# Kernel tuning notes

Measured on AMD Instinct MI355X. Metric: run time of the kernel, lower is better.

The kernel has to match this reference:

```python
import jax, jax.numpy as jnp
import numpy as np

HEAD_SIZE = 64

def setup_inputs() -> dict:
    key = jax.random.key(0)
    kx, kq, kk, kv = jax.random.split(key, 4)
    n_embd = 1024
    x = jax.random.normal(kx, (4, 2048, n_embd), dtype=jnp.float32)
    s = 1.0 / np.sqrt(n_embd)
    Wq = jax.random.normal(kq, (HEAD_SIZE, n_embd), dtype=jnp.float32) * s
    Wk = jax.random.normal(kk, (HEAD_SIZE, n_embd), dtype=jnp.float32) * s
    Wv = jax.random.normal(kv, (HEAD_SIZE, n_embd), dtype=jnp.float32) * s
    return {"x": x, "Wq": Wq, "Wk": Wk, "Wv": Wv}

def reference(x, Wq, Wk, Wv):
    # x: [B, T, C]; W*: [head_size, C] (torch nn.Linear weight layout, y = x @ W.T)
    B, T, C = x.shape
    q = jnp.einsum('btc,hc->bth', x, Wq)  # [B, T, H]
    k = jnp.einsum('btc,hc->bth', x, Wk)
    v = jnp.einsum('btc,hc->bth', x, Wv)
    att = jnp.einsum('bqh,bkh->bqk', q, k) / jnp.sqrt(jnp.float32(HEAD_SIZE))
    causal = jnp.tril(jnp.ones((T, T), dtype=bool))  # [T, T]
    att = jnp.where(causal, att, -jnp.inf)
    att = jax.nn.softmax(att, axis=-1)
    out = jnp.einsum('bqk,bkh->bqh', att, v)  # [B, T, H]
    return out
```

## Files before the change

### kernel.cpp

```cpp
#include <hip/hip_runtime.h>
#include <hip/hip_bf16.h>

#define NB 4
#define TT 2048
#define CC 1024
#define HS 64
#define L2E 1.4426950408889634f

typedef __attribute__((ext_vector_type(8))) short short8;
typedef __attribute__((ext_vector_type(4))) short short4v;
typedef __attribute__((ext_vector_type(4))) float floatx4;
typedef __attribute__((ext_vector_type(2))) float floatx2;

__device__ __forceinline__ short f2bf(float f) {
  union { float f; unsigned u; } x; x.f = f;
  unsigned r = (x.u + 0x7fffu + ((x.u >> 16) & 1u)) >> 16;
  return (short)r;
}

__device__ __forceinline__ short8 pack_bf16x8(floatx4 a, floatx4 b) {
  union { __hip_bfloat162 h[4]; short8 s; } u;
  u.h[0] = __float22bfloat162_rn(make_float2(a[0], a[1]));
  u.h[1] = __float22bfloat162_rn(make_float2(a[2], a[3]));
  u.h[2] = __float22bfloat162_rn(make_float2(b[0], b[1]));
  u.h[3] = __float22bfloat162_rn(make_float2(b[2], b[3]));
  return u.s;
}

__global__ __launch_bounds__(768) void qkv_proj(const float* __restrict__ x,
                                                const float* __restrict__ wq,
                                                const float* __restrict__ wk,
                                                const float* __restrict__ wv,
                                                short* __restrict__ qb,
                                                short* __restrict__ kbuf,
                                                short* __restrict__ vtb) {
  __shared__ __align__(16) short xs[32 * 1024];
  const int tid  = threadIdx.x;
  const int lane = tid & 63;
  const int w    = tid >> 6;
  const int col  = lane & 15;
  const int quad = lane >> 4;
  const int row32 = blockIdx.x * 32;

  const int mat = w >> 2;
  const int ht  = w & 3;
  const float* wsrc = (mat == 0 ? wq : (mat == 1 ? wk : wv))
                      + (size_t)(ht * 16 + col) * CC + quad * 8;

  floatx4 wa = *(const floatx4*)(wsrc);
  floatx4 wc = *(const floatx4*)(wsrc + 4);

#pragma unroll
  for (int i = 0; i < 6; ++i) {
    int c = i * 768 + tid;
    if (c < 4096) {
      int r = c >> 7;
      int k = (c & 127) * 8;
      const float* src = x + (size_t)(row32 + r) * CC + k;
      floatx4 a = *(const floatx4*)src;
      floatx4 b = *(const floatx4*)(src + 4);
      int kb = k >> 5, ko = k & 31;
      *(short8*)(&xs[kb * 1024 + r * 32 + ko]) = pack_bf16x8(a, b);
    }
  }
  __syncthreads();

  floatx4 acc0 = (floatx4){0.f, 0.f, 0.f, 0.f};
  floatx4 acc1 = (floatx4){0.f, 0.f, 0.f, 0.f};

#pragma unroll
  for (int kb = 0; kb < 32; ++kb) {
    short8 bf = pack_bf16x8(wa, wc);
    if (kb < 31) {
      wa = *(const floatx4*)(wsrc + (kb + 1) * 32);
      wc = *(const floatx4*)(wsrc + (kb + 1) * 32 + 4);
    }
    short8 a0 = *(const short8*)(&xs[kb * 1024 + col * 32 + quad * 8]);
    short8 a1 = *(const short8*)(&xs[kb * 1024 + (16 + col) * 32 + quad * 8]);
    acc0 = __builtin_amdgcn_mfma_f32_16x16x32_bf16(a0, bf, acc0, 0, 0, 0);
    acc1 = __builtin_amdgcn_mfma_f32_16x16x32_bf16(a1, bf, acc1, 0, 0, 0);
  }

  const int h = ht * 16 + col;
  if (mat == 2) {
    int b = row32 >> 11;
    int t = (row32 & (TT - 1)) + quad * 4;
    short4v o;
    o[0] = f2bf(acc0[0]); o[1] = f2bf(acc0[1]); o[2] = f2bf(acc0[2]); o[3] = f2bf(acc0[3]);
    *(short4v*)(vtb + (size_t)(b * HS + h) * TT + t) = o;
    o[0] = f2bf(acc1[0]); o[1] = f2bf(acc1[1]); o[2] = f2bf(acc1[2]); o[3] = f2bf(acc1[3]);
    *(short4v*)(vtb + (size_t)(b * HS + h) * TT + t + 16) = o;
  } else {
    short* dst = (mat == 0) ? qb : kbuf;
    float s = (mat == 0) ? 0.125f : 1.0f;
#pragma unroll
    for (int r = 0; r < 4; ++r) {
      dst[(size_t)(row32 + quad * 4 + r) * HS + h]      = f2bf(acc0[r] * s);
      dst[(size_t)(row32 + 16 + quad * 4 + r) * HS + h] = f2bf(acc1[r] * s);
    }
  }
}

#define PST 72

__global__ __launch_bounds__(512) void attn(const short* __restrict__ qb,
                                            const short* __restrict__ kb,
                                            const short* __restrict__ vtb,
                                            float* __restrict__ out) {
  __shared__ __align__(16) short pt[8][2][16 * PST];
  __shared__ float cl[8][16];
  __shared__ __align__(16) float co[8][16][64];

  const int tid  = threadIdx.x;
  const int lane = tid & 63;
  const int w    = tid >> 6;
  const int col  = lane & 15;
  const int quad = lane >> 4;
  const int b  = blockIdx.x >> 7;
  const int qt = blockIdx.x & 127;
  const int t0 = qt * 16;

  const short* qbase = qb + (size_t)(b * TT + t0) * HS;
  const short* kbase = kb + (size_t)b * TT * HS;
  const short* vbase = vtb + (size_t)b * HS * TT;

  short8 qf0 = *(const short8*)(qbase + col * HS + quad * 8);
  short8 qf1 = *(const short8*)(qbase + col * HS + 32 + quad * 8);

  floatx4 oacc[4];
#pragma unroll
  for (int i = 0; i < 4; ++i) oacc[i] = (floatx4){0.f, 0.f, 0.f, 0.f};
  float lsum[4] = {0.f, 0.f, 0.f, 0.f};

  const int Nc = (t0 + 16 + 63) >> 6;

  int parity = 0;
  for (int c = w; c < Nc; c += 8, parity ^= 1) {
    const int kb0 = c * 64;
    const short* kp = kbase + (size_t)kb0 * HS + quad * 8;

    floatx4 st[4];
#pragma unroll
    for (int j = 0; j < 4; ++j) st[j] = (floatx4){0.f, 0.f, 0.f, 0.f};
#pragma unroll
    for (int j = 0; j < 4; ++j) {
      short8 kfa = *(const short8*)(kp + (size_t)(j * 16 + col) * HS);
      short8 kfb = *(const short8*)(kp + (size_t)(j * 16 + col) * HS + 32);
      st[j] = __builtin_amdgcn_mfma_f32_16x16x32_bf16(qf0, kfa, st[j], 0, 0, 0);
      st[j] = __builtin_amdgcn_mfma_f32_16x16x32_bf16(qf1, kfb, st[j], 0, 0, 0);
    }

    if (kb0 + 63 > t0) {
#pragma unroll
      for (int j = 0; j < 4; ++j) {
        int kcol = kb0 + j * 16 + col;
#pragma unroll
        for (int r = 0; r < 4; ++r)
          if (kcol > t0 + quad * 4 + r) st[j][r] = -1e30f;
      }
    }

    float pv[4][4];
#pragma unroll
    for (int j = 0; j < 4; ++j)
#pragma unroll
      for (int r = 0; r < 4; ++r)
        pv[j][r] = exp2f(st[j][r] * L2E);
#pragma unroll
    for (int r = 0; r < 4; ++r)
      lsum[r] += (pv[0][r] + pv[1][r]) + (pv[2][r] + pv[3][r]);

    short* pw = &pt[w][parity][0];
#pragma unroll
    for (int j = 0; j < 4; ++j)
#pragma unroll
      for (int r = 0; r < 4; ++r)
        pw[(quad * 4 + r) * PST + j * 16 + col] = f2bf(pv[j][r]);
    short8 af0 = *(const short8*)(pw + col * PST + quad * 8);
    short8 af1 = *(const short8*)(pw + col * PST + 32 + quad * 8);

#pragma unroll
    for (int ht = 0; ht < 4; ++ht) {
      const short* vp = vbase + (size_t)(ht * 16 + col) * TT + kb0 + quad * 8;
      short8 vf0 = *(const short8*)(vp);
      short8 vf1 = *(const short8*)(vp + 32);
      oacc[ht] = __builtin_amdgcn_mfma_f32_16x16x32_bf16(af0, vf0, oacc[ht], 0, 0, 0);
      oacc[ht] = __builtin_amdgcn_mfma_f32_16x16x32_bf16(af1, vf1, oacc[ht], 0, 0, 0);
    }
  }

#pragma unroll
  for (int r = 0; r < 4; ++r) {
#pragma unroll
    for (int off = 8; off; off >>= 1) lsum[r] += __shfl_xor(lsum[r], off);
    if (col == 0) cl[w][quad * 4 + r] = lsum[r];
#pragma unroll
    for (int ht = 0; ht < 4; ++ht)
      co[w][quad * 4 + r][ht * 16 + col] = oacc[ht][r];
  }
  __syncthreads();

  const int crow = tid >> 5;
  const int ch   = (tid & 31) << 1;
  float L = 0.f;
  floatx2 a = (floatx2){0.f, 0.f};
#pragma unroll
  for (int w2 = 0; w2 < 8; ++w2) {
    L += cl[w2][crow];
    floatx2 ov = *(const floatx2*)&co[w2][crow][ch];
    a[0] += ov[0]; a[1] += ov[1];
  }
  float inv = 1.0f / L;
  floatx2 res = (floatx2){a[0] * inv, a[1] * inv};
  *(floatx2*)(out + (size_t)(b * TT + t0 + crow) * HS + ch) = res;
}

extern "C" void kernel_launch(void* const* d_in, const int* in_sizes, int n_in,
                              void* d_out, int out_size, void* d_ws, size_t ws_size,
                              hipStream_t stream) {
  const float* x  = (const float*)d_in[0];
  const float* wq = (const float*)d_in[1];
  const float* wk = (const float*)d_in[2];
  const float* wv = (const float*)d_in[3];
  float* out = (float*)d_out;

  char* ws = (char*)d_ws;
  short* qbf = (short*)ws;
  short* kbf = (short*)(ws + 1048576);
  short* vtb = (short*)(ws + 2097152);

  hipLaunchKernelGGL(qkv_proj, dim3(256), dim3(768), 0, stream,
                     x, wq, wk, wv, qbf, kbf, vtb);
  hipLaunchKernelGGL(attn, dim3(512), dim3(512), 0, stream, qbf, kbf, vtb, out);
}
```

Measured before the change: 131.0 us.

## Retile QKV projection to 16-row blocks with padded LDS layout

```diff
diff --git a/kernel.cpp b/kernel.cpp
--- a/kernel.cpp
+++ b/kernel.cpp
@@ -27,40 +27,46 @@
   return u.s;
 }
 
-__global__ __launch_bounds__(768) void qkv_proj(const float* __restrict__ x,
+#define XRS 40
+#define XKS 656
+
+__global__ __launch_bounds__(384) void qkv_proj(const float* __restrict__ x,
                                                 const float* __restrict__ wq,
                                                 const float* __restrict__ wk,
                                                 const float* __restrict__ wv,
                                                 short* __restrict__ qb,
                                                 short* __restrict__ kbuf,
                                                 short* __restrict__ vtb) {
-  __shared__ __align__(16) short xs[32 * 1024];
+  __shared__ __align__(16) short xs[32 * XKS];
   const int tid  = threadIdx.x;
   const int lane = tid & 63;
   const int w    = tid >> 6;
   const int col  = lane & 15;
   const int quad = lane >> 4;
-  const int row32 = blockIdx.x * 32;
-
-  const int mat = w >> 2;
-  const int ht  = w & 3;
-  const float* wsrc = (mat == 0 ? wq : (mat == 1 ? wk : wv))
-                      + (size_t)(ht * 16 + col) * CC + quad * 8;
-
-  floatx4 wa = *(const floatx4*)(wsrc);
-  floatx4 wc = *(const floatx4*)(wsrc + 4);
+  const int row16 = blockIdx.x * 16;
+
+  const int mat = w >> 1;
+  const int hp  = w & 1;
+  const float* wmat = (mat == 0 ? wq : (mat == 1 ? wk : wv));
+  const float* wsrc0 = wmat + (size_t)(hp * 32 + col) * CC + quad * 8;
+  const float* wsrc1 = wmat + (size_t)(hp * 32 + 16 + col) * CC + quad * 8;
+
+  floatx4 wa0 = *(const floatx4*)(wsrc0);
+  floatx4 wc0 = *(const floatx4*)(wsrc0 + 4);
+  floatx4 wa1 = *(const floatx4*)(wsrc1);
+  floatx4 wc1 = *(const floatx4*)(wsrc1 + 4);
 
 #pragma unroll
   for (int i = 0; i < 6; ++i) {
-    int c = i * 768 + tid;
-    if (c < 4096) {
+    int c = i * 384 + tid;
+    if (c < 2048) {
       int r = c >> 7;
       int k = (c & 127) * 8;
-      const float* src = x + (size_t)(row32 + r) * CC + k;
+      const float* src = x + (size_t)(row16 + r) * CC + k;
       floatx4 a = *(const floatx4*)src;
       floatx4 b = *(const floatx4*)(src + 4);
       int kb = k >> 5, ko = k & 31;
-      *(short8*)(&xs[kb * 1024 + r * 32 + ko]) = pack_bf16x8(a, b);
+      *(short8*)(&xs[kb * XKS + r * XRS + ko]) = pack_bf16x8(a, b);
     }
   }
   __syncthreads();
@@ -70,33 +76,36 @@
 
 #pragma unroll
   for (int kb = 0; kb < 32; ++kb) {
-    short8 bf = pack_bf16x8(wa, wc);
+    short8 bf0 = pack_bf16x8(wa0, wc0);
+    short8 bf1 = pack_bf16x8(wa1, wc1);
     if (kb < 31) {
-      wa = *(const floatx4*)(wsrc + (kb + 1) * 32);
-      wc = *(const floatx4*)(wsrc + (kb + 1) * 32 + 4);
-    }
-    short8 a0 = *(const short8*)(&xs[kb * 1024 + col * 32 + quad * 8]);
-    short8 a1 = *(const short8*)(&xs[kb * 1024 + (16 + col) * 32 + quad * 8]);
-    acc0 = __builtin_amdgcn_mfma_f32_16x16x32_bf16(a0, bf, acc0, 0, 0, 0);
-    acc1 = __builtin_amdgcn_mfma_f32_16x16x32_bf16(a1, bf, acc1, 0, 0, 0);
-  }
-
-  const int h = ht * 16 + col;
+      wa0 = *(const floatx4*)(wsrc0 + (kb + 1) * 32);
+      wc0 = *(const floatx4*)(wsrc0 + (kb + 1) * 32 + 4);
+      wa1 = *(const floatx4*)(wsrc1 + (kb + 1) * 32);
+      wc1 = *(const floatx4*)(wsrc1 + (kb + 1) * 32 + 4);
+    }
+    short8 a = *(const short8*)(&xs[kb * XKS + col * XRS + quad * 8]);
+    acc0 = __builtin_amdgcn_mfma_f32_16x16x32_bf16(a, bf0, acc0, 0, 0, 0);
+    acc1 = __builtin_amdgcn_mfma_f32_16x16x32_bf16(a, bf1, acc1, 0, 0, 0);
+  }
+
+  const int h0 = (hp * 2) * 16 + col;
+  const int h1 = (hp * 2 + 1) * 16 + col;
   if (mat == 2) {
-    int b = row32 >> 11;
-    int t = (row32 & (TT - 1)) + quad * 4;
+    int b = row16 >> 11;
+    int t = (row16 & (TT - 1)) + quad * 4;
     short4v o;
     o[0] = f2bf(acc0[0]); o[1] = f2bf(acc0[1]); o[2] = f2bf(acc0[2]); o[3] = f2bf(acc0[3]);
-    *(short4v*)(vtb + (size_t)(b * HS + h) * TT + t) = o;
+    *(short4v*)(vtb + (size_t)(b * HS + h0) * TT + t) = o;
     o[0] = f2bf(acc1[0]); o[1] = f2bf(acc1[1]); o[2] = f2bf(acc1[2]); o[3] = f2bf(acc1[3]);
-    *(short4v*)(vtb + (size_t)(b * HS + h) * TT + t + 16) = o;
+    *(short4v*)(vtb + (size_t)(b * HS + h1) * TT + t) = o;
   } else {
     short* dst = (mat == 0) ? qb : kbuf;
     float s = (mat == 0) ? 0.125f : 1.0f;
 #pragma unroll
     for (int r = 0; r < 4; ++r) {
-      dst[(size_t)(row32 + quad * 4 + r) * HS + h]      = f2bf(acc0[r] * s);
-      dst[(size_t)(row32 + 16 + quad * 4 + r) * HS + h] = f2bf(acc1[r] * s);
+      dst[(size_t)(row16 + quad * 4 + r) * HS + h0] = f2bf(acc0[r] * s);
+      dst[(size_t)(row16 + quad * 4 + r) * HS + h1] = f2bf(acc1[r] * s);
     }
   }
 }
@@ -229,7 +238,7 @@
   short* kbf = (short*)(ws + 1048576);
   short* vtb = (short*)(ws + 2097152);
 
-  hipLaunchKernelGGL(qkv_proj, dim3(256), dim3(768), 0, stream,
+  hipLaunchKernelGGL(qkv_proj, dim3(512), dim3(384), 0, stream,
                      x, wq, wk, wv, qbf, kbf, vtb);
   hipLaunchKernelGGL(attn, dim3(512), dim3(512), 0, stream, qbf, kbf, vtb, out);
 }
```

Measured after the change: 151.9 us. 1.16x slower.

## Restructure QKV projection to stream K-chunks of x and weights through double-buffered LDS

Applied to the files above, without the earlier changes.

```diff
diff --git a/kernel.cpp b/kernel.cpp
--- a/kernel.cpp
+++ b/kernel.cpp
@@ -27,6 +27,9 @@
   return u.s;
 }
 
+#define KC 64
+#define WTS 72
+
 __global__ __launch_bounds__(768) void qkv_proj(const float* __restrict__ x,
                                                 const float* __restrict__ wq,
                                                 const float* __restrict__ wk,
@@ -34,69 +37,96 @@
                                                 short* __restrict__ qb,
                                                 short* __restrict__ kbuf,
                                                 short* __restrict__ vtb) {
-  __shared__ __align__(16) short xs[32 * 1024];
+  __shared__ __align__(16) short wt[2][192 * WTS];
+  __shared__ __align__(16) short xs[2][32 * WTS];
+
   const int tid  = threadIdx.x;
   const int lane = tid & 63;
   const int w    = tid >> 6;
   const int col  = lane & 15;
   const int quad = lane >> 4;
   const int row32 = blockIdx.x * 32;
-
-  const int mat = w >> 2;
-  const int ht  = w & 3;
-  const float* wsrc = (mat == 0 ? wq : (mat == 1 ? wk : wv))
-                      + (size_t)(ht * 16 + col) * CC + quad * 8;
-
-  floatx4 wa = *(const floatx4*)(wsrc);
-  floatx4 wc = *(const floatx4*)(wsrc + 4);
-
-#pragma unroll
-  for (int i = 0; i < 6; ++i) {
-    int c = i * 768 + tid;
-    if (c < 4096) {
-      int r = c >> 7;
-      int k = (c & 127) * 8;
-      const float* src = x + (size_t)(row32 + r) * CC + k;
-      floatx4 a = *(const floatx4*)src;
-      floatx4 b = *(const floatx4*)(src + 4);
-      int kb = k >> 5, ko = k & 31;
-      *(short8*)(&xs[kb * 1024 + r * 32 + ko]) = pack_bf16x8(a, b);
-    }
-  }
+  const int rg = w / 6;
+  const int cg = w % 6;
+  const int mat   = cg >> 1;
+  const int hbase = (cg & 1) * 32;
+
+  const int o0 = tid >> 3,        kk0 = (tid & 7) * 8;
+  const int o1 = (768 + tid) >> 3, kk1 = ((768 + tid) & 7) * 8;
+  const float* wsrc0 = (o0 < 64 ? wq + (size_t)o0 * CC
+                                : wk + (size_t)(o0 - 64) * CC) + kk0;
+  const float* wsrc1 = (o1 < 128 ? wk + (size_t)(o1 - 64) * CC
+                                 : wv + (size_t)(o1 - 128) * CC) + kk1;
+  const int xr = tid >> 3, xk = (tid & 7) * 8;
+  const float* xsrc = x + (size_t)(row32 + xr) * CC + xk;
+
+  floatx4 wa0 = *(const floatx4*)(wsrc0);
+  floatx4 wc0 = *(const floatx4*)(wsrc0 + 4);
+  floatx4 wa1 = *(const floatx4*)(wsrc1);
+  floatx4 wc1 = *(const floatx4*)(wsrc1 + 4);
+  floatx4 xa, xc;
+  if (tid < 256) { xa = *(const floatx4*)(xsrc); xc = *(const floatx4*)(xsrc + 4); }
+
+  *(short8*)(&wt[0][o0 * WTS + kk0]) = pack_bf16x8(wa0, wc0);
+  *(short8*)(&wt[0][o1 * WTS + kk1]) = pack_bf16x8(wa1, wc1);
+  if (tid < 256) *(short8*)(&xs[0][xr * WTS + xk]) = pack_bf16x8(xa, xc);
   __syncthreads();
 
   floatx4 acc0 = (floatx4){0.f, 0.f, 0.f, 0.f};
   floatx4 acc1 = (floatx4){0.f, 0.f, 0.f, 0.f};
-
-#pragma unroll
-  for (int kb = 0; kb < 32; ++kb) {
-    short8 bf = pack_bf16x8(wa, wc);
-    if (kb < 31) {
-      wa = *(const floatx4*)(wsrc + (kb + 1) * 32);
-      wc = *(const floatx4*)(wsrc + (kb + 1) * 32 + 4);
-    }
-    short8 a0 = *(const short8*)(&xs[kb * 1024 + col * 32 + quad * 8]);
-    short8 a1 = *(const short8*)(&xs[kb * 1024 + (16 + col) * 32 + quad * 8]);
-    acc0 = __builtin_amdgcn_mfma_f32_16x16x32_bf16(a0, bf, acc0, 0, 0, 0);
-    acc1 = __builtin_amdgcn_mfma_f32_16x16x32_bf16(a1, bf, acc1, 0, 0, 0);
-  }
-
-  const int h = ht * 16 + col;
+  const int arow  = (rg * 16 + col) * WTS + quad * 8;
+  const int brow0 = (cg * 32 + col) * WTS + quad * 8;
+  const int brow1 = (cg * 32 + 16 + col) * WTS + quad * 8;
+
+  for (int ch = 0; ch < 16; ++ch) {
+    const int cur = ch & 1;
+    if (ch < 15) {
+      const int k0 = (ch + 1) * KC;
+      wa0 = *(const floatx4*)(wsrc0 + k0);
+      wc0 = *(const floatx4*)(wsrc0 + k0 + 4);
+      wa1 = *(const floatx4*)(wsrc1 + k0);
+      wc1 = *(const floatx4*)(wsrc1 + k0 + 4);
+      if (tid < 256) {
+        xa = *(const floatx4*)(xsrc + k0);
+        xc = *(const floatx4*)(xsrc + k0 + 4);
+      }
+    }
+#pragma unroll
+    for (int kb2 = 0; kb2 < 2; ++kb2) {
+      short8 a  = *(const short8*)(&xs[cur][arow + kb2 * 32]);
+      short8 b0 = *(const short8*)(&wt[cur][brow0 + kb2 * 32]);
+      short8 b1 = *(const short8*)(&wt[cur][brow1 + kb2 * 32]);
+      acc0 = __builtin_amdgcn_mfma_f32_16x16x32_bf16(a, b0, acc0, 0, 0, 0);
+      acc1 = __builtin_amdgcn_mfma_f32_16x16x32_bf16(a, b1, acc1, 0, 0, 0);
+    }
+    if (ch < 15) {
+      __syncthreads();
+      const int nxt = cur ^ 1;
+      *(short8*)(&wt[nxt][o0 * WTS + kk0]) = pack_bf16x8(wa0, wc0);
+      *(short8*)(&wt[nxt][o1 * WTS + kk1]) = pack_bf16x8(wa1, wc1);
+      if (tid < 256) *(short8*)(&xs[nxt][xr * WTS + xk]) = pack_bf16x8(xa, xc);
+      __syncthreads();
+    }
+  }
+
+  const int h0 = hbase + col;
+  const int h1 = hbase + 16 + col;
   if (mat == 2) {
     int b = row32 >> 11;
-    int t = (row32 & (TT - 1)) + quad * 4;
+    int t = (row32 & (TT - 1)) + rg * 16 + quad * 4;
     short4v o;
     o[0] = f2bf(acc0[0]); o[1] = f2bf(acc0[1]); o[2] = f2bf(acc0[2]); o[3] = f2bf(acc0[3]);
-    *(short4v*)(vtb + (size_t)(b * HS + h) * TT + t) = o;
+    *(short4v*)(vtb + (size_t)(b * HS + h0) * TT + t) = o;
     o[0] = f2bf(acc1[0]); o[1] = f2bf(acc1[1]); o[2] = f2bf(acc1[2]); o[3] = f2bf(acc1[3]);
-    *(short4v*)(vtb + (size_t)(b * HS + h) * TT + t + 16) = o;
+    *(short4v*)(vtb + (size_t)(b * HS + h1) * TT + t) = o;
   } else {
     short* dst = (mat == 0) ? qb : kbuf;
     float s = (mat == 0) ? 0.125f : 1.0f;
 #pragma unroll
     for (int r = 0; r < 4; ++r) {
-      dst[(size_t)(row32 + quad * 4 + r) * HS + h]      = f2bf(acc0[r] * s);
-      dst[(size_t)(row32 + 16 + quad * 4 + r) * HS + h] = f2bf(acc1[r] * s);
+      size_t row = (size_t)(row32 + rg * 16 + quad * 4 + r);
+      dst[row * HS + h0] = f2bf(acc0[r] * s);
+      dst[row * HS + h1] = f2bf(acc1[r] * s);
     }
   }
 }
```

Result: faster. 125.7 us (-4.0%).
